# Kernel optimization log

Hardware: AMD Instinct MI355X
Metric: run time of the kernel (lower is better)

Reference implementation:

```python
import jax, jax.numpy as jnp
import numpy as np

N = 100000   # nodes
E = 3200000  # edges per graph
DP, DA, DF, H, C = 3, 11, 32, 4, 8  # d_p, d_a, d_feat, heads, per-head dim
NEG_SLOPE = 0.2


def gat_conv(x, edge_index, W, att_src, att_dst, bias):
    """PyG GATConv with concat heads and default add_self_loops=True.
    x: [N, DF]; edge_index: [2, E] (row0=src, row1=dst); W: [DF, H*C];
    att_src/att_dst: [H, C]; bias: [H*C]. Returns [N, H*C]."""
    n = x.shape[0]
    loops = jnp.arange(n, dtype=edge_index.dtype)
    src = jnp.concatenate([edge_index[0], loops])
    dst = jnp.concatenate([edge_index[1], loops])
    h = (x @ W).reshape(n, H, C)                       # [N,H,C]
    a_s = jnp.sum(h * att_src[None], axis=-1)          # [N,H]
    a_d = jnp.sum(h * att_dst[None], axis=-1)          # [N,H]
    e = jax.nn.leaky_relu(a_s[src] + a_d[dst], NEG_SLOPE)  # [Etot,H]
    m = jax.ops.segment_max(e, dst, num_segments=n)        # stable softmax per dst
    ex = jnp.exp(e - m[dst])
    den = jax.ops.segment_sum(ex, dst, num_segments=n)
    alpha = ex / den[dst]                               # [Etot,H]
    out = jax.ops.segment_sum(h[src] * alpha[..., None], dst, num_segments=n)
    return out.reshape(n, H * C) + bias


def setup_inputs() -> dict:
    key = jax.random.key(0)
    ks = jax.random.split(key, 32)
    p = lambda k, shp: (jax.random.normal(k, shp, dtype=jnp.float32) * 0.1)
    inp = {
        "F_p_raw": jax.random.normal(ks[0], (N, DP), dtype=jnp.float32),
        "F_a_raw": jax.random.normal(ks[1], (N, DA), dtype=jnp.float32),
        "edge_index_s": jax.random.randint(ks[2], (2, E), 0, N),
        "edge_index_p": jax.random.randint(ks[3], (2, E), 0, N),
        "edge_index_a": jax.random.randint(ks[4], (2, E), 0, N),
        # align linears
        "Wp": p(ks[5], (DP, DF)), "bp": p(ks[6], (DF,)),
        "Wa": p(ks[7], (DA, DF)), "ba": p(ks[8], (DF,)),
        "Ws": p(ks[9], (DP + DA, DF)), "bs": p(ks[10], (DF,)),
        # GAT params per graph
        "Wg_s": p(ks[11], (DF, H * C)), "asrc_s": p(ks[12], (H, C)), "adst_s": p(ks[13], (H, C)), "bg_s": p(ks[14], (H * C,)),
        "Wg_p": p(ks[15], (DF, H * C)), "asrc_p": p(ks[16], (H, C)), "adst_p": p(ks[17], (H, C)), "bg_p": p(ks[18], (H * C,)),
        "Wg_a": p(ks[19], (DF, H * C)), "asrc_a": p(ks[20], (H, C)), "adst_a": p(ks[21], (H, C)), "bg_a": p(ks[22], (H * C,)),
        # fuse MLP
        "W1": p(ks[23], (3 * DF, DF)), "b1": p(ks[24], (DF,)),
        "W2": p(ks[25], (DF, DF)), "b2": p(ks[26], (DF,)),
    }
    return inp


def reference(F_p_raw, F_a_raw, edge_index_s, edge_index_p, edge_index_a,
              Wp, bp, Wa, ba, Ws, bs,
              Wg_s, asrc_s, adst_s, bg_s,
              Wg_p, asrc_p, adst_p, bg_p,
              Wg_a, asrc_a, adst_a, bg_a,
              W1, b1, W2, b2):
    f_s = jnp.concatenate([F_p_raw, F_a_raw], axis=-1) @ Ws + bs
    f_p = F_p_raw @ Wp + bp
    f_a = F_a_raw @ Wa + ba
    h_s = jax.nn.elu(gat_conv(f_s, edge_index_s, Wg_s, asrc_s, adst_s, bg_s))
    h_p = jax.nn.elu(gat_conv(f_p, edge_index_p, Wg_p, asrc_p, adst_p, bg_p))
    h_a = jax.nn.elu(gat_conv(f_a, edge_index_a, Wg_a, asrc_a, adst_a, bg_a))
    h = jnp.concatenate([h_s, h_p, h_a], axis=-1)
    h = jax.nn.relu(h @ W1 + b1)
    return h @ W2 + b2
```

## Files before the change

kernel.cpp:

```cpp
#include <hip/hip_runtime.h>
#include <hip/hip_bf16.h>
#include <stdint.h>

typedef __hip_bfloat16 bf16;

__device__ __forceinline__ float b2f(bf16 v){ return __bfloat162float(v); }

__device__ __forceinline__ uint16_t f2b(float x){
  uint32_t u = __float_as_uint(x);
  return (uint16_t)((u + 0x7FFFu + ((u >> 16) & 1u)) >> 16);
}

#define DSTS_PER_BKT 128
#define BKT_SHIFT 7
#define CAP 6144
#define BIN_IT 32
#define MAXB 1024
#define ROWS_PER_WAVE (DSTS_PER_BKT / 4)
#define CURPAD 16

struct CvtTab {
  const void* src[24];
  int n[24];
  int off[24];
};

__global__ __launch_bounds__(256) void k_detect(const void* __restrict__ sample,
                                                int* __restrict__ flag)
{
  __shared__ int bad;
  if (threadIdx.x == 0) bad = 0;
  __syncthreads();
  const unsigned short* u = (const unsigned short*)sample;
  int lbad = 0;
  for (int k = threadIdx.x; k < 1024; k += 256) {
    unsigned short b = u[k];
    unsigned e = (b >> 7) & 0xFFu;
    if (e >= 141u || (e <= 90u && (b & 0x7FFFu) != 0)) lbad = 1;
  }
  if (lbad) atomicOr(&bad, 1);
  __syncthreads();
  if (threadIdx.x == 0) flag[0] = (bad == 0) ? 1 : 0;
}

__global__ __launch_bounds__(256) void k_convert(CvtTab tab, const int* __restrict__ flag,
                                                 float* __restrict__ dst, int total)
{
  const bool isb = (*flag) != 0;
  for (int t = blockIdx.x * 256 + threadIdx.x; t < total; t += gridDim.x * 256) {
    int a = 0;
    while (a < 23 && t >= tab.off[a] + tab.n[a]) ++a;
    int j = t - tab.off[a];
    float v = isb ? b2f(((const bf16*)tab.src[a])[j])
                  : ((const float*)tab.src[a])[j];
    dst[t] = v;
  }
}

__global__ __launch_bounds__(256) void k_node(
  const float* __restrict__ cFp, const float* __restrict__ cFa,
  const float* __restrict__ cWp, const float* __restrict__ cbp,
  const float* __restrict__ cWa, const float* __restrict__ cba,
  const float* __restrict__ cWs, const float* __restrict__ cbs,
  const float* __restrict__ cWg0, const float* __restrict__ cAs0, const float* __restrict__ cAd0,
  const float* __restrict__ cWg1, const float* __restrict__ cAs1, const float* __restrict__ cAd1,
  const float* __restrict__ cWg2, const float* __restrict__ cAs2, const float* __restrict__ cAd2,
  uint32_t* __restrict__ hgb, uint16_t* __restrict__ asb, float* __restrict__ a_d,
  float* __restrict__ den, float* __restrict__ agg, int N)
{
  __shared__ float sWs[14*32];
  __shared__ float sWp[3*32];
  __shared__ float sWa[11*32];
  __shared__ float sb[3][32];
  __shared__ float sWg[3][32*32];
  __shared__ float sA[3][2][32];
  const int tid = threadIdx.x;
  for (int t = tid; t < 14*32; t += 256) sWs[t] = cWs[t];
  for (int t = tid; t < 3*32;  t += 256) sWp[t] = cWp[t];
  for (int t = tid; t < 11*32; t += 256) sWa[t] = cWa[t];
  if (tid < 32) {
    sb[0][tid] = cbs[tid]; sb[1][tid] = cbp[tid]; sb[2][tid] = cba[tid];
    sA[0][0][tid] = cAs0[tid]; sA[0][1][tid] = cAd0[tid];
    sA[1][0][tid] = cAs1[tid]; sA[1][1][tid] = cAd1[tid];
    sA[2][0][tid] = cAs2[tid]; sA[2][1][tid] = cAd2[tid];
  }
  for (int t = tid; t < 32*32; t += 256) {
    sWg[0][t] = cWg0[t]; sWg[1][t] = cWg1[t]; sWg[2][t] = cWg2[t];
  }
  __syncthreads();

  const int i = blockIdx.x * 256 + tid;
  if (i >= N) return;

  float xp[3], xa[11];
  #pragma unroll
  for (int k = 0; k < 3; ++k)  xp[k] = cFp[i*3 + k];
  #pragma unroll
  for (int k = 0; k < 11; ++k) xa[k] = cFa[i*11 + k];

  for (int g = 0; g < 3; ++g) {
    float f[32];
    if (g == 0) {
      #pragma unroll
      for (int j = 0; j < 32; ++j) {
        float acc = sb[0][j];
        #pragma unroll
        for (int k = 0; k < 3; ++k)  acc += xp[k] * sWs[k*32 + j];
        #pragma unroll
        for (int k = 0; k < 11; ++k) acc += xa[k] * sWs[(3+k)*32 + j];
        f[j] = acc;
      }
    } else if (g == 1) {
      #pragma unroll
      for (int j = 0; j < 32; ++j) {
        float acc = sb[1][j];
        #pragma unroll
        for (int k = 0; k < 3; ++k) acc += xp[k] * sWp[k*32 + j];
        f[j] = acc;
      }
    } else {
      #pragma unroll
      for (int j = 0; j < 32; ++j) {
        float acc = sb[2][j];
        #pragma unroll
        for (int k = 0; k < 11; ++k) acc += xa[k] * sWa[k*32 + j];
        f[j] = acc;
      }
    }

    const float* Wg = sWg[g];
    float hv[32];
    #pragma unroll
    for (int j = 0; j < 32; ++j) {
      float acc = 0.f;
      #pragma unroll
      for (int k = 0; k < 32; ++k) acc += f[k] * Wg[k*32 + j];
      hv[j] = acc;
    }

    float asv[4], adv[4], exv[4];
    #pragma unroll
    for (int h = 0; h < 4; ++h) {
      float s0 = 0.f, s1 = 0.f;
      #pragma unroll
      for (int c = 0; c < 8; ++c) {
        s0 += hv[h*8 + c] * sA[g][0][h*8 + c];
        s1 += hv[h*8 + c] * sA[g][1][h*8 + c];
      }
      asv[h] = s0; adv[h] = s1;
      float e = s0 + s1;
      e = e > 0.f ? e : 0.2f * e;
      exv[h] = __expf(e);
    }

    const size_t row = (size_t)g * N + i;
    uint32_t* hp = hgb + row * 16;
    #pragma unroll
    for (int q = 0; q < 4; ++q) {
      uint4 u;
      u.x = (uint32_t)f2b(hv[q*8+0]) | ((uint32_t)f2b(hv[q*8+1]) << 16);
      u.y = (uint32_t)f2b(hv[q*8+2]) | ((uint32_t)f2b(hv[q*8+3]) << 16);
      u.z = (uint32_t)f2b(hv[q*8+4]) | ((uint32_t)f2b(hv[q*8+5]) << 16);
      u.w = (uint32_t)f2b(hv[q*8+6]) | ((uint32_t)f2b(hv[q*8+7]) << 16);
      *(uint4*)(hp + q*4) = u;
    }
    *(ushort4*)(asb + row * 4) =
        make_ushort4(f2b(asv[0]), f2b(asv[1]), f2b(asv[2]), f2b(asv[3]));

    float4* agp = (float4*)(agg + row * 32);
    #pragma unroll
    for (int q = 0; q < 8; ++q) {
      float ex = exv[q >> 1];
      agp[q] = make_float4(ex*hv[q*4+0], ex*hv[q*4+1], ex*hv[q*4+2], ex*hv[q*4+3]);
    }
    *(float4*)(a_d + row*4) = make_float4(adv[0], adv[1], adv[2], adv[3]);
    *(float4*)(den + row*4) = make_float4(exv[0], exv[1], exv[2], exv[3]);
  }
}

__global__ __launch_bounds__(256) void k_hist(
  const int* __restrict__ ei0, const int* __restrict__ ei1, const int* __restrict__ ei2,
  int* __restrict__ gb_hist, int NBPG, int E)
{
  const int g = blockIdx.y;
  const int* __restrict__ ei = (g == 0) ? ei0 : (g == 1 ? ei1 : ei2);
  __shared__ int hist[MAXB];
  for (int t = threadIdx.x; t < NBPG; t += 256) hist[t] = 0;
  __syncthreads();
  const int base = blockIdx.x * (256 * BIN_IT);
  #pragma unroll
  for (int k = 0; k < BIN_IT; ++k) {
    int idx = base + k * 256 + threadIdx.x;
    if (idx < E) atomicAdd(&hist[ei[E + idx] >> BKT_SHIFT], 1);
  }
  __syncthreads();
  for (int t = threadIdx.x; t < NBPG; t += 256)
    if (hist[t]) atomicAdd(&gb_hist[g * NBPG + t], hist[t]);
}

#define SCAN_IPT 16
__global__ __launch_bounds__(256) void k_bscan(
  const int* __restrict__ gb_hist, int* __restrict__ boff, int* __restrict__ cur, int nb)
{
  __shared__ int s[256];
  const int base = threadIdx.x * SCAN_IPT;
  int v[SCAN_IPT]; int sum = 0;
  #pragma unroll
  for (int k = 0; k < SCAN_IPT; ++k) {
    int i = base + k; int x = (i < nb) ? gb_hist[i] : 0; v[k] = x; sum += x;
  }
  s[threadIdx.x] = sum;
  __syncthreads();
  for (int d = 1; d < 256; d <<= 1) {
    int t = (threadIdx.x >= d) ? s[threadIdx.x - d] : 0;
    __syncthreads();
    s[threadIdx.x] += t;
    __syncthreads();
  }
  int run = s[threadIdx.x] - sum;
  #pragma unroll
  for (int k = 0; k < SCAN_IPT; ++k) {
    int i = base + k;
    if (i < nb) { boff[i] = run; cur[(size_t)i * CURPAD] = run; run += v[k]; }
  }
  if (threadIdx.x == 255) boff[nb] = s[255];
}

__global__ __launch_bounds__(256) void k_bin(
  const int* __restrict__ ei0, const int* __restrict__ ei1, const int* __restrict__ ei2,
  int* __restrict__ cur, int* __restrict__ bins, int NBPG, int E)
{
  const int g = blockIdx.y;
  const int* __restrict__ ei = (g == 0) ? ei0 : (g == 1 ? ei1 : ei2);
  __shared__ int hist[MAXB];
  __shared__ int bbase[MAXB];
  const int tid = threadIdx.x;
  for (int t = tid; t < NBPG; t += 256) hist[t] = 0;
  __syncthreads();
  const int base = blockIdx.x * (256 * BIN_IT);
  int pk[BIN_IT];
  #pragma unroll
  for (int k = 0; k < BIN_IT; ++k) {
    int idx = base + k * 256 + tid;
    if (idx < E) {
      int d = ei[E + idx];
      int loc = atomicAdd(&hist[d >> BKT_SHIFT], 1);
      pk[k] = (loc << 17) | d;
    } else pk[k] = -1;
  }
  __syncthreads();
  for (int t = tid; t < NBPG; t += 256) {
    int c = hist[t];
    bbase[t] = c ? atomicAdd(&cur[(size_t)(g * NBPG + t) * CURPAD], c) : 0;
  }
  __syncthreads();
  #pragma unroll
  for (int k = 0; k < BIN_IT; ++k) {
    int p = pk[k];
    if (p >= 0) {
      int d   = p & 0x1FFFF;
      int loc = p >> 17;
      int idx = base + k * 256 + tid;
      int src = ei[idx];
      bins[bbase[d >> BKT_SHIFT] + loc] = ((d & (DSTS_PER_BKT - 1)) << 17) | src;
    }
  }
}

__global__ __launch_bounds__(256) void k_vgather(
  const int* __restrict__ boff, const int* __restrict__ bins,
  const uint32_t* __restrict__ hgb, const uint16_t* __restrict__ asb,
  const float* __restrict__ a_d,
  float* __restrict__ den, float* __restrict__ agg, int NBPG, int N)
{
  __shared__ int sorted[CAP];
  __shared__ int soff[DSTS_PER_BKT + 1];
  __shared__ int scnt[DSTS_PER_BKT];
  __shared__ int sscan[DSTS_PER_BKT];
  const int g  = blockIdx.y;
  const int b  = blockIdx.x;
  const int gb = g * NBPG + b;
  const int s0 = boff[gb];
  const int n  = boff[gb + 1] - s0;
  const int tid = threadIdx.x;
  const int wave = tid >> 6;
  const int lane = tid & 63;
  const int sub  = lane >> 4;
  const int l16  = lane & 15;
  const int h    = l16 >> 2;
  const size_t gbase = (size_t)g * N;
  const int dst0 = b * DSTS_PER_BKT;

  for (int cbase = 0; cbase < n; cbase += CAP) {
    const int m = min(CAP, n - cbase);
    if (tid < DSTS_PER_BKT) scnt[tid] = 0;
    __syncthreads();
    for (int i = tid; i < m; i += 256)
      atomicAdd(&scnt[(bins[s0 + cbase + i] >> 17) & (DSTS_PER_BKT - 1)], 1);
    __syncthreads();
    if (tid < DSTS_PER_BKT) sscan[tid] = scnt[tid];
    __syncthreads();
    for (int d = 1; d < DSTS_PER_BKT; d <<= 1) {
      int t = 0;
      if (tid < DSTS_PER_BKT && tid >= d) t = sscan[tid - d];
      __syncthreads();
      if (tid < DSTS_PER_BKT) sscan[tid] += t;
      __syncthreads();
    }
    if (tid < DSTS_PER_BKT) {
      int ex = sscan[tid] - scnt[tid];
      soff[tid] = ex;
      scnt[tid] = ex;
    }
    if (tid == 0) soff[DSTS_PER_BKT] = m;
    __syncthreads();
    for (int i = tid; i < m; i += 256) {
      int p = bins[s0 + cbase + i];
      int pos = atomicAdd(&scnt[(p >> 17) & (DSTS_PER_BKT - 1)], 1);
      sorted[pos] = p & 0x1FFFF;
    }
    __syncthreads();

    const int rbeg = wave * ROWS_PER_WAVE;
    for (int rl = rbeg; rl < rbeg + ROWS_PER_WAVE; ++rl) {
      const int dst = dst0 + rl;
      if (dst >= N) break;
      const int cs = soff[rl], ce = soff[rl + 1];
      const size_t row = gbase + dst;
      const float ad = a_d[row * 4 + h];
      float ax = 0.f, ay = 0.f, w = 0.f;
      for (int c = cs + sub; c < ce; c += 16) {
        const int i0 = c        < ce ? sorted[c]      : -1;
        const int i1 = (c + 4)  < ce ? sorted[c + 4]  : -1;
        const int i2 = (c + 8)  < ce ? sorted[c + 8]  : -1;
        const int i3 = (c + 12) < ce ? sorted[c + 12] : -1;
        const int p0 = i0 < 0 ? 0 : i0;
        const int p1 = i1 < 0 ? 0 : i1;
        const int p2 = i2 < 0 ? 0 : i2;
        const int p3 = i3 < 0 ? 0 : i3;
        const uint32_t u0 = hgb[(gbase + p0) * 16 + l16];
        const uint32_t u1 = hgb[(gbase + p1) * 16 + l16];
        const uint32_t u2 = hgb[(gbase + p2) * 16 + l16];
        const uint32_t u3 = hgb[(gbase + p3) * 16 + l16];
        const uint16_t t0 = asb[(gbase + p0) * 4 + h];
        const uint16_t t1 = asb[(gbase + p1) * 4 + h];
        const uint16_t t2 = asb[(gbase + p2) * 4 + h];
        const uint16_t t3 = asb[(gbase + p3) * 4 + h];
        float e0 = __uint_as_float((uint32_t)t0 << 16) + ad; e0 = e0 > 0.f ? e0 : 0.2f * e0;
        float e1 = __uint_as_float((uint32_t)t1 << 16) + ad; e1 = e1 > 0.f ? e1 : 0.2f * e1;
        float e2 = __uint_as_float((uint32_t)t2 << 16) + ad; e2 = e2 > 0.f ? e2 : 0.2f * e2;
        float e3 = __uint_as_float((uint32_t)t3 << 16) + ad; e3 = e3 > 0.f ? e3 : 0.2f * e3;
        const float w0 = i0 >= 0 ? __expf(e0) : 0.f;
        const float w1 = i1 >= 0 ? __expf(e1) : 0.f;
        const float w2 = i2 >= 0 ? __expf(e2) : 0.f;
        const float w3 = i3 >= 0 ? __expf(e3) : 0.f;
        ax += w0 * __uint_as_float(u0 << 16);
        ay += w0 * __uint_as_float(u0 & 0xFFFF0000u);
        ax += w1 * __uint_as_float(u1 << 16);
        ay += w1 * __uint_as_float(u1 & 0xFFFF0000u);
        ax += w2 * __uint_as_float(u2 << 16);
        ay += w2 * __uint_as_float(u2 & 0xFFFF0000u);
        ax += w3 * __uint_as_float(u3 << 16);
        ay += w3 * __uint_as_float(u3 & 0xFFFF0000u);
        w += w0 + w1 + w2 + w3;
      }
      ax += __shfl_xor(ax, 16); ay += __shfl_xor(ay, 16); w += __shfl_xor(w, 16);
      ax += __shfl_xor(ax, 32); ay += __shfl_xor(ay, 32); w += __shfl_xor(w, 32);
      if (sub == 0) {
        float2* ap = (float2*)(agg + row * 32) + l16;
        float2 sv = *ap;
        sv.x += ax; sv.y += ay;
        *ap = sv;
        if ((l16 & 3) == 0) den[row * 4 + h] += w;
      }
    }
    __syncthreads();
  }
}

__global__ __launch_bounds__(256) void k_final(
  const float* __restrict__ den, const float* __restrict__ agg,
  const float* __restrict__ cbg0, const float* __restrict__ cbg1, const float* __restrict__ cbg2,
  const float* __restrict__ cW1, const float* __restrict__ cb1,
  const float* __restrict__ cW2, const float* __restrict__ cb2,
  const int* __restrict__ flag, void* __restrict__ out, int N)
{
  __shared__ float sW1[96*32];
  __shared__ float sW2[32*32];
  __shared__ float sb1[32], sb2[32], sbg[3][32];
  const int tid = threadIdx.x;
  for (int t = tid; t < 96*32; t += 256) sW1[t] = cW1[t];
  for (int t = tid; t < 32*32; t += 256) sW2[t] = cW2[t];
  if (tid < 32) {
    sb1[tid] = cb1[tid]; sb2[tid] = cb2[tid];
    sbg[0][tid] = cbg0[tid]; sbg[1][tid] = cbg1[tid]; sbg[2][tid] = cbg2[tid];
  }
  __syncthreads();

  const int i = blockIdx.x * 256 + tid;
  if (i >= N) return;

  float h96[96];
  #pragma unroll
  for (int g = 0; g < 3; ++g) {
    const size_t row = (size_t)g * N + i;
    float4 d4 = *(const float4*)(den + row * 4);
    float invs[4] = {1.f/d4.x, 1.f/d4.y, 1.f/d4.z, 1.f/d4.w};
    const float4* av = (const float4*)(agg + row * 32);
    #pragma unroll
    for (int q = 0; q < 8; ++q) {
      float4 a4 = av[q];
      float iv = invs[q >> 1];
      float vals[4] = {a4.x, a4.y, a4.z, a4.w};
      #pragma unroll
      for (int k = 0; k < 4; ++k) {
        float v = vals[k] * iv + sbg[g][q*4 + k];
        v = v > 0.f ? v : (__expf(v) - 1.f);
        h96[g*32 + q*4 + k] = v;
      }
    }
  }

  float h1[32];
  #pragma unroll
  for (int j = 0; j < 32; ++j) {
    float acc = sb1[j];
    #pragma unroll
    for (int k = 0; k < 96; ++k) acc += h96[k] * sW1[k*32 + j];
    h1[j] = acc > 0.f ? acc : 0.f;
  }

  const bool isb = (*flag) != 0;
  #pragma unroll
  for (int j = 0; j < 32; ++j) {
    float acc = sb2[j];
    #pragma unroll
    for (int k = 0; k < 32; ++k) acc += h1[k] * sW2[k*32 + j];
    if (isb) ((bf16*)out)[(size_t)i*32 + j] = __float2bfloat16(acc);
    else     ((float*)out)[(size_t)i*32 + j] = acc;
  }
}

extern "C" void kernel_launch(void* const* d_in, const int* in_sizes, int n_in,
                              void* d_out, int out_size, void* d_ws, size_t ws_size,
                              hipStream_t stream)
{
  const int N = in_sizes[0] / 3;
  const int E = in_sizes[2] / 2;
  const int NBPG = (N + DSTS_PER_BKT - 1) / DSTS_PER_BKT;
  const int nb = 3 * NBPG;

  float* ws  = (float*)d_ws;
  int* flag  = (int*)d_ws;
  float* cvt = ws + 64;

  static const int order[24] = {1, 0,
    5, 6, 7, 8, 9, 10,
    11, 12, 13, 14,
    15, 16, 17, 18,
    19, 20, 21, 22,
    23, 24, 25, 26};
  CvtTab tab;
  int off0 = 0;
  for (int a = 0; a < 24; ++a) {
    tab.src[a] = d_in[order[a]];
    tab.n[a]   = in_sizes[order[a]];
    tab.off[a] = off0;
    off0 += tab.n[a];
  }
  const int total = off0;

  float* P[24];
  for (int a = 0; a < 24; ++a) P[a] = cvt + tab.off[a];
  float *cFa = P[0],  *cFp = P[1];
  float *cWp = P[2],  *cbp = P[3],  *cWa = P[4],  *cba = P[5],  *cWs = P[6], *cbs = P[7];
  float *cWg0 = P[8],  *cAs0 = P[9],  *cAd0 = P[10], *cbg0 = P[11];
  float *cWg1 = P[12], *cAs1 = P[13], *cAd1 = P[14], *cbg1 = P[15];
  float *cWg2 = P[16], *cAs2 = P[17], *cAd2 = P[18], *cbg2 = P[19];
  float *cW1 = P[20], *cb1 = P[21], *cW2 = P[22], *cb2 = P[23];

  int pad = (4 - (total & 3)) & 3;
  float* big = cvt + total + pad;
  const size_t n3 = (size_t)3 * N;
  float* agg  = big;
  float* a_d  = agg + n3 * 32;
  float* den  = a_d + n3 * 4;
  uint32_t* hgb = (uint32_t*)(den + n3 * 4);
  uint16_t* asb = (uint16_t*)(hgb + n3 * 16);
  int* gb_hist = (int*)(asb + n3 * 4);
  int* boff    = gb_hist + nb;
  int* cur     = boff + nb + 1;
  int* bins    = cur + (size_t)nb * CURPAD + CURPAD;

  const int ebx = (E + 256 * BIN_IT - 1) / (256 * BIN_IT);

  k_detect<<<1, 256, 0, stream>>>(d_in[1], flag);
  k_convert<<<2048, 256, 0, stream>>>(tab, flag, cvt, total);
  k_node<<<(N + 255) / 256, 256, 0, stream>>>(
      cFp, cFa, cWp, cbp, cWa, cba, cWs, cbs,
      cWg0, cAs0, cAd0, cWg1, cAs1, cAd1, cWg2, cAs2, cAd2,
      hgb, asb, a_d, den, agg, N);

  hipMemsetAsync(gb_hist, 0, nb * sizeof(int), stream);

  dim3 ge((unsigned)ebx, 3, 1);
  k_hist<<<ge, 256, 0, stream>>>(
      (const int*)d_in[2], (const int*)d_in[3], (const int*)d_in[4], gb_hist, NBPG, E);
  k_bscan<<<1, 256, 0, stream>>>(gb_hist, boff, cur, nb);
  k_bin<<<ge, 256, 0, stream>>>(
      (const int*)d_in[2], (const int*)d_in[3], (const int*)d_in[4], cur, bins, NBPG, E);

  dim3 gg((unsigned)NBPG, 3, 1);
  k_vgather<<<gg, 256, 0, stream>>>(boff, bins, hgb, asb, a_d, den, agg, NBPG, N);

  k_final<<<(N + 255) / 256, 256, 0, stream>>>(
      den, agg, cbg0, cbg1, cbg2, cW1, cb1, cW2, cb2, flag, d_out, N);
}
```

Measured before the change: 514.8 us.

## Stage binned edges in shared memory before coalesced global write-out

The binning kernel now scatters packed edge entries into a shared-memory staging buffer ordered by a block-local prefix scan of bucket counts. Each wave then copies whole bucket runs to global memory with contiguous lanes, so the writes coalesce instead of being random scattered stores. This adds a block scan, an extra pass through shared memory and about 40KB of LDS per block, which may lower occupancy.

```diff
diff --git a/kernel.cpp b/kernel.cpp
--- a/kernel.cpp
+++ b/kernel.cpp
@@ -232,38 +232,78 @@
 {
   const int g = blockIdx.y;
   const int* __restrict__ ei = (g == 0) ? ei0 : (g == 1 ? ei1 : ei2);
+  __shared__ int sp[256 * BIN_IT];
   __shared__ int hist[MAXB];
-  __shared__ int bbase[MAXB];
+  __shared__ int soff[MAXB];
+  __shared__ int grun[MAXB];
+  __shared__ int s[256];
   const int tid = threadIdx.x;
   for (int t = tid; t < NBPG; t += 256) hist[t] = 0;
   __syncthreads();
   const int base = blockIdx.x * (256 * BIN_IT);
+
   int pk[BIN_IT];
   #pragma unroll
   for (int k = 0; k < BIN_IT; ++k) {
     int idx = base + k * 256 + tid;
     if (idx < E) {
       int d = ei[E + idx];
-      int loc = atomicAdd(&hist[d >> BKT_SHIFT], 1);
-      pk[k] = (loc << 17) | d;
+      int b = d >> BKT_SHIFT;
+      int loc = atomicAdd(&hist[b], 1);
+      pk[k] = (b << 20) | (loc << 7) | (d & (DSTS_PER_BKT - 1));
     } else pk[k] = -1;
   }
   __syncthreads();
+
+  {
+    const int sbase = tid * 4;
+    int v[4]; int sum = 0;
+    #pragma unroll
+    for (int j = 0; j < 4; ++j) {
+      int i = sbase + j; int x = (i < NBPG) ? hist[i] : 0; v[j] = x; sum += x;
+    }
+    s[tid] = sum;
+    __syncthreads();
+    for (int d = 1; d < 256; d <<= 1) {
+      int t = (tid >= d) ? s[tid - d] : 0;
+      __syncthreads();
+      s[tid] += t;
+      __syncthreads();
+    }
+    int run = s[tid] - sum;
+    #pragma unroll
+    for (int j = 0; j < 4; ++j) {
+      int i = sbase + j;
+      if (i < NBPG) { soff[i] = run; run += v[j]; }
+    }
+  }
   for (int t = tid; t < NBPG; t += 256) {
     int c = hist[t];
-    bbase[t] = c ? atomicAdd(&cur[(size_t)(g * NBPG + t) * CURPAD], c) : 0;
-  }
-  __syncthreads();
+    grun[t] = c ? atomicAdd(&cur[(size_t)(g * NBPG + t) * CURPAD], c) : 0;
+  }
+  __syncthreads();
+
   #pragma unroll
   for (int k = 0; k < BIN_IT; ++k) {
     int p = pk[k];
     if (p >= 0) {
-      int d   = p & 0x1FFFF;
-      int loc = p >> 17;
       int idx = base + k * 256 + tid;
       int src = ei[idx];
-      bins[bbase[d >> BKT_SHIFT] + loc] = ((d & (DSTS_PER_BKT - 1)) << 17) | src;
-    }
+      int b   = p >> 20;
+      int loc = (p >> 7) & 0x1FFF;
+      int dl  = p & (DSTS_PER_BKT - 1);
+      sp[soff[b] + loc] = (dl << 17) | src;
+    }
+  }
+  __syncthreads();
+
+  const int wave = tid >> 6, lane = tid & 63;
+  for (int b = wave; b < NBPG; b += 4) {
+    const int c  = hist[b];
+    const int gb_ = grun[b];
+    const int ls = soff[b];
+    for (int i = lane; i < c; i += 64)
+      bins[gb_ + i] = sp[ls + i];
   }
 }
 
```

Result: faster. 499.4 us (-3.0%).
